# Performance work log

Hardware: AMD Instinct MI355X
Metric: run time of the kernel (lower is better)

## Reference

```python
import jax, jax.numpy as jnp
import numpy as np

# Static config (init_kwargs)
H = 56; W = 56; C = 256; NH = 8; WS = 7; SS = 3
HD = C // NH
SCALE = HD ** -0.5
N = WS * WS                      # tokens per window = 49
NW = (H // WS) * (W // WS)       # windows per image = 64
HIDDEN = int(C * 4.0)
EPS = 1e-5


def _rel_pos_index():
    coords = np.stack(np.meshgrid(np.arange(WS), np.arange(WS), indexing='ij')).reshape(2, -1)
    rel = coords[:, :, None] - coords[:, None, :]          # [2, N, N]
    rel = rel.transpose(1, 2, 0).astype(np.int64)          # [N, N, 2]
    rel[:, :, 0] += WS - 1
    rel[:, :, 1] += WS - 1
    rel[:, :, 0] *= 2 * WS - 1
    return rel.sum(-1).reshape(-1)                         # [N*N]


def _attn_mask():
    # (0 / -100) mask for the shifted-window configuration, [NW, N, N]
    img = np.zeros([H, W])
    cnt = 0
    for hs in (slice(0, -WS), slice(-WS, -SS), slice(-SS, None)):
        for ws in (slice(0, -WS), slice(-WS, -SS), slice(-SS, None)):
            img[hs, ws] = cnt
            cnt += 1
    mw = img.reshape(H // WS, WS, W // WS, WS).transpose(0, 2, 1, 3).reshape(-1, N)
    diff = mw[:, None, :] - mw[:, :, None]                 # [NW, N, N]
    return np.where(diff != 0, -100.0, 0.0).astype(np.float32)


_REL_IDX = _rel_pos_index()
_MASK = _attn_mask()


def _ln(x, g, b):
    mu = jnp.mean(x, axis=-1, keepdims=True)
    var = jnp.mean((x - mu) ** 2, axis=-1, keepdims=True)
    return (x - mu) * jax.lax.rsqrt(var + EPS) * g + b


def setup_inputs() -> dict:
    key = jax.random.key(0)
    ks = jax.random.split(key, 16)
    B = 32
    s = 0.02
    return {
        'x': jax.random.normal(ks[0], (B, H * W, C), dtype=jnp.float32),
        'gamma1': jnp.ones((C,), jnp.float32),
        'beta1': jnp.zeros((C,), jnp.float32),
        'qkv_w': jax.random.normal(ks[1], (C, 3 * C), jnp.float32) * s,
        'qkv_b': jnp.zeros((3 * C,), jnp.float32),
        'proj_w': jax.random.normal(ks[2], (C, C), jnp.float32) * s,
        'proj_b': jnp.zeros((C,), jnp.float32),
        'rpb_table': jax.random.normal(ks[3], ((2 * WS - 1) * (2 * WS - 1), NH), jnp.float32) * s,
        'gamma2': jnp.ones((C,), jnp.float32),
        'beta2': jnp.zeros((C,), jnp.float32),
        'fc1_w': jax.random.normal(ks[4], (C, HIDDEN), jnp.float32) * s,
        'fc1_b': jnp.zeros((HIDDEN,), jnp.float32),
        'fc2_w': jax.random.normal(ks[5], (HIDDEN, C), jnp.float32) * s,
        'fc2_b': jnp.zeros((C,), jnp.float32),
    }


def reference(x, gamma1, beta1, qkv_w, qkv_b, proj_w, proj_b, rpb_table,
              gamma2, beta2, fc1_w, fc1_b, fc2_w, fc2_b):
    B = x.shape[0]
    y = _ln(x, gamma1, beta1).reshape(B, H, W, C)
    # cyclic shift
    y = jnp.roll(y, (-SS, -SS), axis=(1, 2))
    # window partition -> [B*NW, N, C]
    win = y.reshape(B, H // WS, WS, W // WS, WS, C)
    win = win.transpose(0, 1, 3, 2, 4, 5).reshape(-1, N, C)
    # qkv projection, split heads
    qkv = (win @ qkv_w + qkv_b).reshape(-1, N, 3, NH, HD).transpose(2, 0, 3, 1, 4)
    q, k, v = qkv[0] * SCALE, qkv[1], qkv[2]            # [B*NW, NH, N, HD]
    attn = jnp.einsum('bhnd,bhmd->bhnm', q, k)          # [B*NW, NH, N, N]
    # gathered relative position bias
    bias = rpb_table[jnp.asarray(_REL_IDX)].reshape(N, N, NH).transpose(2, 0, 1)
    attn = attn + bias[None]
    # shift mask
    mask = jnp.asarray(_MASK)                           # [NW, N, N]
    attn = attn.reshape(B, NW, NH, N, N) + mask[None, :, None]
    attn = jax.nn.softmax(attn.reshape(-1, NH, N, N), axis=-1)
    o = jnp.einsum('bhnm,bhmd->bnhd', attn, v).reshape(-1, N, C)
    o = o @ proj_w + proj_b
    # window reverse + reverse shift
    o = o.reshape(B, H // WS, W // WS, WS, WS, C).transpose(0, 1, 3, 2, 4, 5).reshape(B, H, W, C)
    o = jnp.roll(o, (SS, SS), axis=(1, 2)).reshape(B, H * W, C)
    x = x + o
    # MLP block
    y = _ln(x, gamma2, beta2)
    y = jax.nn.gelu(y @ fc1_w + fc1_b, approximate=False) @ fc2_w + fc2_b
    return x + y
```

## Files before the change

### kernel.cpp

```cpp
#include <hip/hip_runtime.h>
#include <hip/hip_bf16.h>
#include <math.h>


typedef __bf16 bf16_t;
typedef __bf16 bf16x4 __attribute__((ext_vector_type(4)));
typedef __bf16 bf16x8 __attribute__((ext_vector_type(8)));
typedef float f32x4 __attribute__((ext_vector_type(4)));

#define AS1 __attribute__((address_space(1)))
#define AS3 __attribute__((address_space(3)))

__device__ __forceinline__ void gload_lds16(const bf16_t* g, bf16_t* l) {
  __builtin_amdgcn_global_load_lds((AS1 void*)g, (AS3 void*)l, 16, 0, 0);
}

__global__ void transpose_cast3(const float* __restrict__ qkv_w,
                                const float* __restrict__ proj_w,
                                const float* __restrict__ fc1_w,
                                bf16_t* __restrict__ qkvWt,
                                bf16_t* __restrict__ projWt,
                                bf16_t* __restrict__ fc1Wt) {
  int idx = blockIdx.x * 256 + threadIdx.x;
  const float* w;
  bf16_t* wt;
  int N;
  if (blockIdx.y == 0) { w = qkv_w; wt = qkvWt; N = 768; }
  else if (blockIdx.y == 1) { w = proj_w; wt = projWt; N = 256; }
  else { w = fc1_w; wt = fc1Wt; N = 1024; }
  if (idx < N * 256) {
    int n = idx >> 8, k = idx & 255;
    wt[idx] = (bf16_t)w[(size_t)k * N + n];
  }
}

__global__ void transpose_cast(const float* __restrict__ w, bf16_t* __restrict__ wt,
                               int K, int N) {
  int idx = blockIdx.x * 256 + threadIdx.x;
  if (idx < N * K) {
    int n = idx / K, k = idx - n * K;
    wt[idx] = (bf16_t)w[(size_t)k * N + n];
  }
}

__global__ void build_bm(const float* __restrict__ rpb, float* __restrict__ bm) {
  int t = blockIdx.x, h = blockIdx.y;
  int wr = (t & 2) ? 7 : 0, wc = (t & 1) ? 7 : 0;
  for (int e = threadIdx.x; e < 4096; e += 256) {
    int r = e >> 6, c = e & 63;
    float v;
    if (c >= 49) {
      v = -30000.f;
    } else if (r >= 49) {
      v = 0.f;
    } else {
      int r1 = r / 7, c1 = r - r1 * 7;
      int r2 = c / 7, c2 = c - r2 * 7;
      v = rpb[((r1 - r2 + 6) * 13 + (c1 - c2 + 6)) * 8 + h];
      int hp = wr * 7 + r1, wp = wc * 7 + c1;
      int hq = wr * 7 + r2, wq = wc * 7 + c2;
      int ri = (hp < 49 ? 0 : (hp < 53 ? 1 : 2)) * 3 + (wp < 49 ? 0 : (wp < 53 ? 1 : 2));
      int rj = (hq < 49 ? 0 : (hq < 53 ? 1 : 2)) * 3 + (wq < 49 ? 0 : (wq < 53 ? 1 : 2));
      if (ri != rj) v -= 100.f;
    }
    bm[((size_t)(t * 8 + h) * 64 + r) * 64 + c] = v;
  }
}

__global__ __launch_bounds__(256)
void ln_cast(const float* __restrict__ src, const float* __restrict__ gamma,
             const float* __restrict__ beta, bf16_t* __restrict__ dst, int windowed) {
  int row = blockIdx.x * 4 + (threadIdx.x >> 6);
  int lane = threadIdx.x & 63;
  size_t srow;
  if (windowed) {
    int w = row / 49, t = row - w * 49;
    int img = w >> 6, wi = w & 63;
    int wr = wi >> 3, wc = wi & 7;
    int rr = t / 7, cc = t - rr * 7;
    int h = wr * 7 + rr + 3; if (h >= 56) h -= 56;
    int ww = wc * 7 + cc + 3; if (ww >= 56) ww -= 56;
    srow = (size_t)img * 3136 + h * 56 + ww;
  } else {
    srow = row;
  }
  float4 v = *(const float4*)(src + srow * 256 + lane * 4);
  float s = v.x + v.y + v.z + v.w;
  float s2 = v.x * v.x + v.y * v.y + v.z * v.z + v.w * v.w;
#pragma unroll
  for (int off = 32; off > 0; off >>= 1) {
    s += __shfl_xor(s, off);
    s2 += __shfl_xor(s2, off);
  }
  float mu = s * (1.0f / 256.0f);
  float rs = rsqrtf(s2 * (1.0f / 256.0f) - mu * mu + 1e-5f);
  float4 g = *(const float4*)(gamma + lane * 4);
  float4 b = *(const float4*)(beta + lane * 4);
  bf16x4 o;
  o[0] = (bf16_t)((v.x - mu) * rs * g.x + b.x);
  o[1] = (bf16_t)((v.y - mu) * rs * g.y + b.y);
  o[2] = (bf16_t)((v.z - mu) * rs * g.z + b.z);
  o[3] = (bf16_t)((v.w - mu) * rs * g.w + b.w);
  *(bf16x4*)(dst + (size_t)row * 256 + lane * 4) = o;
}

template <int MODE>
__global__ __launch_bounds__(256)
void gemm_bt(const bf16_t* __restrict__ A, const bf16_t* __restrict__ Bt,
             const float* __restrict__ bias,
             bf16_t* Cbf, float* Cf, const float* Res,
             int M, int N, int K, int nblk) {
  __shared__ __align__(16) bf16_t As[128 * 32];
  __shared__ __align__(16) bf16_t Bs[128 * 32];
  const int tid = threadIdx.x;
  const int lane = tid & 63;
  const int wave = tid >> 6;
  const int wm = wave & 1, wn = wave >> 1;
  const int bid = blockIdx.x;
  const int m_idx = bid / nblk;
  const int n_idx = bid - m_idx * nblk;
  const int m0 = m_idx * 128;
  const int n0 = n_idx * 128;

  f32x4 acc[4][4];
#pragma unroll
  for (int i = 0; i < 4; i++)
#pragma unroll
    for (int j = 0; j < 4; j++) acc[i][j] = f32x4{0.f, 0.f, 0.f, 0.f};

  const bf16_t* Ag = A + (size_t)m0 * K;
  const bf16_t* Bg = Bt + (size_t)n0 * K;
  const int lr = lane & 15;
  const int kq = (lane >> 4) * 8;

  for (int k0 = 0; k0 < K; k0 += 32) {
#pragma unroll
    for (int it = 0; it < 2; it++) {
      int slot = it * 256 + tid;
      int row = slot >> 2;
      int ko = (slot & 3) << 3;
      bf16_t* ldsA = As + (it * 256 + wave * 64) * 8;
      bf16_t* ldsB = Bs + (it * 256 + wave * 64) * 8;
      gload_lds16(Ag + (size_t)row * K + k0 + ko, ldsA);
      gload_lds16(Bg + (size_t)row * K + k0 + ko, ldsB);
    }
    __syncthreads();
    bf16x8 af[4], bfr[4];
#pragma unroll
    for (int i = 0; i < 4; i++) {
      af[i]  = *(const bf16x8*)(As + (wm * 64 + i * 16 + lr) * 32 + kq);
      bfr[i] = *(const bf16x8*)(Bs + (wn * 64 + i * 16 + lr) * 32 + kq);
    }
#pragma unroll
    for (int i = 0; i < 4; i++)
#pragma unroll
      for (int j = 0; j < 4; j++)
        acc[i][j] = __builtin_amdgcn_mfma_f32_16x16x32_bf16(af[i], bfr[j], acc[i][j], 0, 0, 0);
    __syncthreads();
  }

  const int quad = lane >> 4;
#pragma unroll
  for (int i = 0; i < 4; i++) {
    int rbase = m0 + wm * 64 + i * 16 + quad * 4;
#pragma unroll
    for (int j = 0; j < 4; j++) {
      int col = n0 + wn * 64 + j * 16 + lr;
      float bi = bias[col];
#pragma unroll
      for (int r = 0; r < 4; r++) {
        int row = rbase + r;
        float v = acc[i][j][r] + bi;
        if (MODE == 0) {
          Cbf[(size_t)row * N + col] = (bf16_t)v;
        } else {
          int w = row / 49, t = row - w * 49;
          int img = w >> 6, wi = w & 63;
          int wr = wi >> 3, wc = wi & 7;
          int rr = t / 7, cc = t - rr * 7;
          int h = wr * 7 + rr + 3; if (h >= 56) h -= 56;
          int ww2 = wc * 7 + cc + 3; if (ww2 >= 56) ww2 -= 56;
          size_t idx = ((size_t)img * 3136 + h * 56 + ww2) * 256 + col;
          Cf[idx] = v + Res[idx];
        }
      }
    }
  }
}

__global__ __launch_bounds__(256)
void attn_mfma(const bf16_t* __restrict__ qkv, const float* __restrict__ bm,
               bf16_t* __restrict__ o) {
  __shared__ __align__(16) bf16_t Ps[64 * 72];
  __shared__ __align__(16) bf16_t Vt[32 * 72];
  const int w = blockIdx.x, h = blockIdx.y;
  const int tid = threadIdx.x;
  const int lane = tid & 63, wv = tid >> 6;
  const int lr = lane & 15, quad = lane >> 4;
  const int wi = w & 63;
  const int mtype = (((wi >> 3) == 7) ? 2 : 0) | (((wi & 7) == 7) ? 1 : 0);
  const bf16_t* base = qkv + (size_t)w * 49 * 768 + h * 32;

  bf16x8 zero8;
#pragma unroll
  for (int z = 0; z < 8; z++) zero8[z] = (bf16_t)0.f;

  {
    int tok = tid >> 2, d8 = (tid & 3) * 8;
    bf16x8 v8 = zero8;
    if (tok < 49) v8 = *(const bf16x8*)(base + (size_t)tok * 768 + 512 + d8);
#pragma unroll
    for (int z = 0; z < 8; z++) Vt[(d8 + z) * 72 + tok] = v8[z];
  }
  __syncthreads();

  const int mrow = 16 * wv + lr;
  bf16x8 aq = zero8;
  if (mrow < 49) aq = *(const bf16x8*)(base + (size_t)mrow * 768 + quad * 8);
  f32x4 s[4];
#pragma unroll
  for (int j = 0; j < 4; j++) {
    int nrow = 16 * j + lr;
    bf16x8 bk = zero8;
    if (nrow < 49) bk = *(const bf16x8*)(base + (size_t)nrow * 768 + 256 + quad * 8);
    s[j] = __builtin_amdgcn_mfma_f32_16x16x32_bf16(aq, bk, f32x4{0.f, 0.f, 0.f, 0.f}, 0, 0, 0);
  }

  const float* bmb = bm + ((size_t)(mtype * 8 + h) * 64 + 16 * wv) * 64;
  float inv[4];
#pragma unroll
  for (int reg = 0; reg < 4; reg++) {
    int rl = quad * 4 + reg;
    float v0[4];
    float mx = -1e30f;
#pragma unroll
    for (int j = 0; j < 4; j++) {
      float v = s[j][reg] * 0.17677669529663689f + bmb[rl * 64 + 16 * j + lr];
      v0[j] = v;
      mx = fmaxf(mx, v);
    }
#pragma unroll
    for (int off = 8; off > 0; off >>= 1) mx = fmaxf(mx, __shfl_xor(mx, off));
    float sum = 0.f;
#pragma unroll
    for (int j = 0; j < 4; j++) {
      float e = __expf(v0[j] - mx);
      v0[j] = e;
      sum += e;
    }
#pragma unroll
    for (int off = 8; off > 0; off >>= 1) sum += __shfl_xor(sum, off);
    inv[reg] = 1.0f / sum;
#pragma unroll
    for (int j = 0; j < 4; j++)
      Ps[(16 * wv + rl) * 72 + 16 * j + lr] = (bf16_t)v0[j];
  }

  f32x4 oacc[2];
  oacc[0] = f32x4{0.f, 0.f, 0.f, 0.f};
  oacc[1] = f32x4{0.f, 0.f, 0.f, 0.f};
#pragma unroll
  for (int kk = 0; kk < 2; kk++) {
    bf16x8 ap = *(const bf16x8*)(Ps + (16 * wv + lr) * 72 + kk * 32 + quad * 8);
#pragma unroll
    for (int n = 0; n < 2; n++) {
      bf16x8 bv = *(const bf16x8*)(Vt + (16 * n + lr) * 72 + kk * 32 + quad * 8);
      oacc[n] = __builtin_amdgcn_mfma_f32_16x16x32_bf16(ap, bv, oacc[n], 0, 0, 0);
    }
  }
#pragma unroll
  for (int n = 0; n < 2; n++) {
#pragma unroll
    for (int reg = 0; reg < 4; reg++) {
      int row = 16 * wv + quad * 4 + reg;
      if (row < 49) {
        int d = 16 * n + lr;
        o[((size_t)w * 49 + row) * 256 + h * 32 + d] = (bf16_t)(oacc[n][reg] * inv[reg]);
      }
    }
  }
}

__global__ __launch_bounds__(256, 3)
void fused_mlp(const bf16_t* __restrict__ y2, const bf16_t* __restrict__ W1t,
               const float* __restrict__ b1, const bf16_t* __restrict__ W2t,
               const float* __restrict__ b2, float* __restrict__ out) {
  __shared__ __align__(16) bf16_t Ws[16384];
  __shared__ __align__(16) bf16_t Hs[4 * 16 * 136];
  const int tid = threadIdx.x;
  const int lane = tid & 63, wave = tid >> 6;
  const int lr = lane & 15, quad = lane >> 4;
  const int m0 = blockIdx.x * 64;
  bf16_t* HsW = Hs + wave * (16 * 136);

  const bf16_t* Arow = y2 + (size_t)(m0 + 16 * wave + lr) * 256;
  bf16x8 aF[2][4];
#pragma unroll
  for (int ks = 0; ks < 2; ks++)
#pragma unroll
    for (int kk = 0; kk < 4; kk++)
      aF[ks][kk] = *(const bf16x8*)(Arow + ks * 128 + kk * 32 + quad * 8);

  f32x4 acc2[16];
#pragma unroll
  for (int n = 0; n < 16; n++) acc2[n] = f32x4{0.f, 0.f, 0.f, 0.f};

  for (int hc = 0; hc < 8; hc++) {
    f32x4 acc1[8];
#pragma unroll
    for (int j = 0; j < 8; j++) acc1[j] = f32x4{0.f, 0.f, 0.f, 0.f};

    for (int ks = 0; ks < 2; ks++) {
      __syncthreads();
#pragma unroll
      for (int kk = 0; kk < 4; kk++) {
#pragma unroll
        for (int it = 0; it < 2; it++) {
          int row = it * 64 + wave * 16 + (lane >> 2);
          int k8 = lane & 3;
          const bf16_t* src = W1t + (size_t)(hc * 128 + row) * 256
                              + ks * 128 + kk * 32 + k8 * 8;
          gload_lds16(src, Ws + kk * 4096 + (it * 64 + wave * 16) * 32);
        }
      }
      __syncthreads();
#pragma unroll
      for (int kk = 0; kk < 4; kk++) {
#pragma unroll
        for (int j = 0; j < 8; j++) {
          bf16x8 b = *(const bf16x8*)(Ws + kk * 4096 + (16 * j + lr) * 32 + quad * 8);
          acc1[j] = __builtin_amdgcn_mfma_f32_16x16x32_bf16(aF[ks][kk], b, acc1[j], 0, 0, 0);
        }
      }
    }
#pragma unroll
    for (int j = 0; j < 8; j++) {
      float bias1 = b1[hc * 128 + 16 * j + lr];
#pragma unroll
      for (int reg = 0; reg < 4; reg++) {
        float v = acc1[j][reg] + bias1;
        v = 0.5f * v * (1.0f + erff(v * 0.70710678118654752f));
        HsW[(4 * quad + reg) * 136 + 16 * j + lr] = (bf16_t)v;
      }
    }
    for (int ks2 = 0; ks2 < 2; ks2++) {
      __syncthreads();
#pragma unroll
      for (int kk = 0; kk < 2; kk++) {
#pragma unroll
        for (int it = 0; it < 4; it++) {
          int row = it * 64 + wave * 16 + (lane >> 2);
          int k8 = lane & 3;
          const bf16_t* src = W2t + (size_t)row * 1024
                              + hc * 128 + ks2 * 64 + kk * 32 + k8 * 8;
          gload_lds16(src, Ws + kk * 8192 + (it * 64 + wave * 16) * 32);
        }
      }
      __syncthreads();
#pragma unroll
      for (int kk = 0; kk < 2; kk++) {
        bf16x8 ah = *(const bf16x8*)(HsW + lr * 136 + ks2 * 64 + kk * 32 + quad * 8);
#pragma unroll
        for (int n = 0; n < 16; n++) {
          bf16x8 bw = *(const bf16x8*)(Ws + kk * 8192 + (16 * n + lr) * 32 + quad * 8);
          acc2[n] = __builtin_amdgcn_mfma_f32_16x16x32_bf16(ah, bw, acc2[n], 0, 0, 0);
        }
      }
    }
  }

#pragma unroll
  for (int n = 0; n < 16; n++) {
    int col = 16 * n + lr;
    float bi = b2[col];
#pragma unroll
    for (int reg = 0; reg < 4; reg++) {
      int row = m0 + 16 * wave + 4 * quad + reg;
      size_t idx = (size_t)row * 256 + col;
      out[idx] = acc2[n][reg] + bi + out[idx];
    }
  }
}

extern "C" void kernel_launch(void* const* d_in, const int* in_sizes, int n_in,
                              void* d_out, int out_size, void* d_ws, size_t ws_size,
                              hipStream_t stream) {
  const float* x      = (const float*)d_in[0];
  const float* g1     = (const float*)d_in[1];
  const float* b1     = (const float*)d_in[2];
  const float* qkv_w  = (const float*)d_in[3];
  const float* qkv_b  = (const float*)d_in[4];
  const float* proj_w = (const float*)d_in[5];
  const float* proj_b = (const float*)d_in[6];
  const float* rpb    = (const float*)d_in[7];
  const float* g2     = (const float*)d_in[8];
  const float* b2     = (const float*)d_in[9];
  const float* fc1_w  = (const float*)d_in[10];
  const float* fc1_b  = (const float*)d_in[11];
  const float* fc2_w  = (const float*)d_in[12];
  const float* fc2_b  = (const float*)d_in[13];
  float* out = (float*)d_out;
  char* ws = (char*)d_ws;

  bf16_t* xw   = (bf16_t*)ws;
  bf16_t* qkv  = (bf16_t*)(ws + 51380224);
  bf16_t* ow   = (bf16_t*)(ws + 205520896);
  bf16_t* y2   = xw;
  bf16_t* qkvWt  = (bf16_t*)(ws + 256901120);
  bf16_t* projWt = qkvWt + 768 * 256;
  bf16_t* fc1Wt  = projWt + 256 * 256;
  bf16_t* fc2Wt  = fc1Wt + 1024 * 256;
  float*  bm     = (float*)fc2Wt;

  transpose_cast3<<<dim3(1024, 3), 256, 0, stream>>>(qkv_w, proj_w, fc1_w,
                                                     qkvWt, projWt, fc1Wt);
  build_bm<<<dim3(4, 8), 256, 0, stream>>>(rpb, bm);

  ln_cast<<<25088, 256, 0, stream>>>(x, g1, b1, xw, 1);
  gemm_bt<0><<<784 * 6, 256, 0, stream>>>(xw, qkvWt, qkv_b, qkv, nullptr, nullptr,
                                          100352, 768, 256, 6);
  attn_mfma<<<dim3(2048, 8), 256, 0, stream>>>(qkv, bm, ow);
  transpose_cast<<<(256 * 1024 + 255) / 256, 256, 0, stream>>>(fc2_w, fc2Wt, 1024, 256);
  gemm_bt<3><<<784 * 2, 256, 0, stream>>>(ow, projWt, proj_b, nullptr, out, x,
                                          100352, 256, 256, 2);
  ln_cast<<<25088, 256, 0, stream>>>(out, g2, b2, y2, 0);
  fused_mlp<<<1568, 256, 0, stream>>>(y2, fc1Wt, fc1_b, fc2Wt, fc2_b, out);
}
```

Measured before the change: 766.3 us.

## Triple-buffer MLP weight tiles with swizzled LDS layout and prefetch pipeline

Restructures the fused MLP weight streaming into a 64-stage, three-buffer pipeline. Loads for stage s+2 are issued before computing stage s, with explicit vmcnt waits and raw barriers replacing the load-sync-compute pattern. The LDS tiles use an XOR swizzle to avoid bank conflicts, and the fc1 bias is staged into shared memory. LDS use rises to about 70 KB, so launch bounds drop from 3 to 2 blocks per CU, trading occupancy for overlap. The hand-written waitcnt and barrier sequencing is fragile.

```diff
diff --git a/kernel.cpp b/kernel.cpp
--- a/kernel.cpp
+++ b/kernel.cpp
@@ -281,18 +281,21 @@
   }
 }
 
-__global__ __launch_bounds__(256, 3)
+__global__ __launch_bounds__(256, 2)
 void fused_mlp(const bf16_t* __restrict__ y2, const bf16_t* __restrict__ W1t,
                const float* __restrict__ b1, const bf16_t* __restrict__ W2t,
                const float* __restrict__ b2, float* __restrict__ out) {
-  __shared__ __align__(16) bf16_t Ws[16384];
+  __shared__ __align__(16) bf16_t Ws[3 * 8192];
   __shared__ __align__(16) bf16_t Hs[4 * 16 * 136];
+  __shared__ float b1s[1024];
   const int tid = threadIdx.x;
   const int lane = tid & 63, wave = tid >> 6;
   const int lr = lane & 15, quad = lane >> 4;
   const int m0 = blockIdx.x * 64;
   bf16_t* HsW = Hs + wave * (16 * 136);
 
+  for (int i = tid; i < 1024; i += 256) b1s[i] = b1[i];
+
   const bf16_t* Arow = y2 + (size_t)(m0 + 16 * wave + lr) * 256;
   bf16x8 aF[2][4];
 #pragma unroll
@@ -305,37 +308,68 @@
 #pragma unroll
   for (int n = 0; n < 16; n++) acc2[n] = f32x4{0.f, 0.f, 0.f, 0.f};
 
+  const int rowA = wave * 8 + (lane >> 3);
+  const int koffA = ((((lane & 7) << 4) ^ ((lane >> 3) << 4)) >> 1);
+  const int rowB = wave * 16 + (lane >> 2);
+  const int koffB = ((((lane & 3) << 4) ^ (((lane >> 2) & 3) << 4)) >> 1);
+  const int swzA = (lr & 7) << 4;
+  const int swzB = (lr & 3) << 4;
+
+  auto issue = [&](int s2, int buf) {
+    int hc2 = s2 >> 3, sub2 = s2 & 3;
+    bf16_t* dst = Ws + buf * 8192;
+    if (((s2 >> 2) & 1) == 0) {
+#pragma unroll
+      for (int it = 0; it < 4; it++)
+        gload_lds16(W1t + (size_t)(hc2 * 128 + it * 32 + rowA) * 256 + sub2 * 64 + koffA,
+                    dst + it * 2048 + wave * 512);
+    } else {
+#pragma unroll
+      for (int it = 0; it < 4; it++)
+        gload_lds16(W2t + (size_t)(it * 64 + rowB) * 1024 + hc2 * 128 + sub2 * 32 + koffB,
+                    dst + it * 2048 + wave * 512);
+    }
+  };
+
+  asm volatile("s_waitcnt vmcnt(0) lgkmcnt(0)" ::: "memory");
+  issue(0, 0);
+  issue(1, 1);
+  int cur = 0, nxt = 1, nx2 = 2;
+
   for (int hc = 0; hc < 8; hc++) {
     f32x4 acc1[8];
 #pragma unroll
     for (int j = 0; j < 8; j++) acc1[j] = f32x4{0.f, 0.f, 0.f, 0.f};
 
-    for (int ks = 0; ks < 2; ks++) {
-      __syncthreads();
-#pragma unroll
-      for (int kk = 0; kk < 4; kk++) {
-#pragma unroll
-        for (int it = 0; it < 2; it++) {
-          int row = it * 64 + wave * 16 + (lane >> 2);
-          int k8 = lane & 3;
-          const bf16_t* src = W1t + (size_t)(hc * 128 + row) * 256
-                              + ks * 128 + kk * 32 + k8 * 8;
-          gload_lds16(src, Ws + kk * 4096 + (it * 64 + wave * 16) * 32);
+#pragma unroll
+    for (int sub = 0; sub < 4; sub++) {
+      const int s = hc * 8 + sub;
+      if (s + 2 < 64) issue(s + 2, nx2);
+      if (s < 62)       asm volatile("s_waitcnt vmcnt(8)" ::: "memory");
+      else if (s == 62) asm volatile("s_waitcnt vmcnt(4)" ::: "memory");
+      else              asm volatile("s_waitcnt vmcnt(0)" ::: "memory");
+      __builtin_amdgcn_s_barrier();
+      __builtin_amdgcn_sched_barrier(0);
+      const char* WsC = (const char*)(Ws + cur * 8192);
+#pragma unroll
+      for (int kk2 = 0; kk2 < 2; kk2++) {
+        bf16x8 aa = aF[sub >> 1][(sub & 1) * 2 + kk2];
+#pragma unroll
+        for (int j = 0; j < 8; j++) {
+          bf16x8 b = *(const bf16x8*)(WsC + (16 * j + lr) * 128 +
+                                      ((kk2 * 64 + quad * 16) ^ swzA));
+          acc1[j] = __builtin_amdgcn_mfma_f32_16x16x32_bf16(aa, b, acc1[j], 0, 0, 0);
         }
       }
-      __syncthreads();
-#pragma unroll
-      for (int kk = 0; kk < 4; kk++) {
-#pragma unroll
-        for (int j = 0; j < 8; j++) {
-          bf16x8 b = *(const bf16x8*)(Ws + kk * 4096 + (16 * j + lr) * 32 + quad * 8);
-          acc1[j] = __builtin_amdgcn_mfma_f32_16x16x32_bf16(aF[ks][kk], b, acc1[j], 0, 0, 0);
-        }
-      }
-    }
+      asm volatile("s_waitcnt lgkmcnt(0)" ::: "memory");
+      __builtin_amdgcn_sched_barrier(0);
+      __builtin_amdgcn_s_barrier();
+      int t = cur; cur = nxt; nxt = nx2; nx2 = t;
+    }
+
 #pragma unroll
     for (int j = 0; j < 8; j++) {
-      float bias1 = b1[hc * 128 + 16 * j + lr];
+      float bias1 = b1s[hc * 128 + 16 * j + lr];
 #pragma unroll
       for (int reg = 0; reg < 4; reg++) {
         float v = acc1[j][reg] + bias1;
@@ -343,29 +377,28 @@
         HsW[(4 * quad + reg) * 136 + 16 * j + lr] = (bf16_t)v;
       }
     }
-    for (int ks2 = 0; ks2 < 2; ks2++) {
-      __syncthreads();
-#pragma unroll
-      for (int kk = 0; kk < 2; kk++) {
-#pragma unroll
-        for (int it = 0; it < 4; it++) {
-          int row = it * 64 + wave * 16 + (lane >> 2);
-          int k8 = lane & 3;
-          const bf16_t* src = W2t + (size_t)row * 1024
-                              + hc * 128 + ks2 * 64 + kk * 32 + k8 * 8;
-          gload_lds16(src, Ws + kk * 8192 + (it * 64 + wave * 16) * 32);
-        }
+
+#pragma unroll
+    for (int sub = 0; sub < 4; sub++) {
+      const int s = hc * 8 + 4 + sub;
+      if (s + 2 < 64) issue(s + 2, nx2);
+      if (s < 62)       asm volatile("s_waitcnt vmcnt(8)" ::: "memory");
+      else if (s == 62) asm volatile("s_waitcnt vmcnt(4)" ::: "memory");
+      else              asm volatile("s_waitcnt vmcnt(0)" ::: "memory");
+      __builtin_amdgcn_s_barrier();
+      __builtin_amdgcn_sched_barrier(0);
+      const char* WsC = (const char*)(Ws + cur * 8192);
+      bf16x8 ah = *(const bf16x8*)(HsW + lr * 136 + sub * 32 + quad * 8);
+#pragma unroll
+      for (int n = 0; n < 16; n++) {
+        bf16x8 bw = *(const bf16x8*)(WsC + (16 * n + lr) * 64 +
+                                     ((quad * 16) ^ swzB));
+        acc2[n] = __builtin_amdgcn_mfma_f32_16x16x32_bf16(ah, bw, acc2[n], 0, 0, 0);
       }
-      __syncthreads();
-#pragma unroll
-      for (int kk = 0; kk < 2; kk++) {
-        bf16x8 ah = *(const bf16x8*)(HsW + lr * 136 + ks2 * 64 + kk * 32 + quad * 8);
-#pragma unroll
-        for (int n = 0; n < 16; n++) {
-          bf16x8 bw = *(const bf16x8*)(Ws + kk * 8192 + (16 * n + lr) * 32 + quad * 8);
-          acc2[n] = __builtin_amdgcn_mfma_f32_16x16x32_bf16(ah, bw, acc2[n], 0, 0, 0);
-        }
-      }
+      asm volatile("s_waitcnt lgkmcnt(0)" ::: "memory");
+      __builtin_amdgcn_sched_barrier(0);
+      __builtin_amdgcn_s_barrier();
+      int t = cur; cur = nxt; nxt = nx2; nx2 = t;
     }
   }
 
```

Measured after the change: 806.9 us. 5.3% more time.
